# Kernel optimization log

Hardware: AMD Instinct MI355X
Metric: run time of the kernel (lower is better)

The kernel has to match this reference:

```python
import jax, jax.numpy as jnp
import numpy as np
import math

B, LC, LQ, D = 64, 1024, 128, 128


def setup_inputs() -> dict:
    key = jax.random.key(0)
    k1, k2, k3, k4, k5 = jax.random.split(key, 5)
    c_rep = jax.random.normal(k1, (B, LC, D), dtype=jnp.float32)
    q_rep = jax.random.normal(k2, (B, LQ, D), dtype=jnp.float32)
    c_mask = jax.random.randint(k3, (B, LC), 0, 2, dtype=jnp.int32)
    q_mask = jax.random.randint(k4, (B, LQ), 0, 2, dtype=jnp.int32)
    lim = math.sqrt(1.0 / D)
    w = jax.random.uniform(k5, (3 * D,), dtype=jnp.float32, minval=-lim, maxval=lim)
    return {"c_rep": c_rep, "q_rep": q_rep, "c_mask": c_mask, "q_mask": q_mask, "w": w}


def _mask_logits(t, m):
    # mask == 1 means masked (matches original: target*(1-mask) + mask*-1e30)
    return t * (1.0 - m) + m * (-1e30)


def reference(c_rep, q_rep, c_mask, q_mask, w):
    d = c_rep.shape[-1]
    w1, w2, w3 = w[:d], w[d:2 * d], w[2 * d:]
    # Trilinear similarity S[b,i,j] = <ct,w1> + <qt,w2> + <ct*qt,w3>
    # computed without materializing the [B,Lc,Lq,3D] concat tensor.
    S = (c_rep @ w1)[:, :, None] \
        + (q_rep @ w2)[:, None, :] \
        + jnp.einsum('bid,bjd->bij', c_rep * w3, q_rep)  # [B, Lc, Lq]
    qm = q_mask[:, None, :].astype(S.dtype)  # [B, 1, Lq]
    cm = c_mask[:, :, None].astype(S.dtype)  # [B, Lc, 1]
    S1 = jax.nn.softmax(_mask_logits(S, qm), axis=2)  # softmax over query dim
    S2 = jax.nn.softmax(_mask_logits(S, cm), axis=1)  # softmax over context dim
    A = jnp.einsum('bij,bjd->bid', S1, q_rep)  # [B, Lc, D]
    # B_att = S1 @ S2^T @ c_rep, associated right-first to avoid [B,Lc,Lc]
    T = jnp.einsum('bkj,bkd->bjd', S2, c_rep)  # [B, Lq, D]
    B_att = jnp.einsum('bij,bjd->bid', S1, T)  # [B, Lc, D]
    out = jnp.concatenate([c_rep, A, c_rep * A, c_rep * B_att], axis=2)  # [B, Lc, 4D]
    # dropout is identity at inference
    return out
```

## Files before the change

### kernel.cpp

```cpp
#include <hip/hip_runtime.h>
#include <hip/hip_bf16.h>
#include <cstdint>
#include <cstddef>

#define B_   64
#define LC_  1024
#define LQ_  128
#define D_   128

typedef __bf16 bf16;
typedef bf16  bf16x8 __attribute__((ext_vector_type(8)));
typedef bf16  bf16x4 __attribute__((ext_vector_type(4)));
typedef float f32x4  __attribute__((ext_vector_type(4)));

__device__ __forceinline__ f32x4 mfma16(bf16x8 a, bf16x8 b, f32x4 c) {
  return __builtin_amdgcn_mfma_f32_16x16x32_bf16(a, b, c, 0, 0, 0);
}

__global__ __launch_bounds__(256) void k0c(const float* __restrict__ c, const float* __restrict__ w,
                                           float* __restrict__ cw1, bf16* __restrict__ cw3,
                                           bf16* __restrict__ cT) {
  __shared__ float w1s[128];
  __shared__ float w3s[128];
  __shared__ bf16  ctile[128 * 132];
  const int b = blockIdx.y, ks = blockIdx.x;
  const int k0 = ks * 128;
  const int t = threadIdx.x;
  if (t < 128) { w1s[t] = w[t]; w3s[t] = w[256 + t]; }
  __syncthreads();
  {
    const int r = t >> 1, d0 = (t & 1) * 64;
    const float* crow = c + ((size_t)(b * LC_ + k0 + r) * D_ + d0);
    bf16* orow = cw3 + ((size_t)(b * LC_ + k0 + r) * D_ + d0);
    float dot = 0.f;
#pragma unroll
    for (int v = 0; v < 8; ++v) {
      const float4 f0 = ((const float4*)crow)[v * 2 + 0];
      const float4 f1 = ((const float4*)crow)[v * 2 + 1];
      const int dd = d0 + v * 8;
      dot += f0.x * w1s[dd + 0] + f0.y * w1s[dd + 1] + f0.z * w1s[dd + 2] + f0.w * w1s[dd + 3]
           + f1.x * w1s[dd + 4] + f1.y * w1s[dd + 5] + f1.z * w1s[dd + 6] + f1.w * w1s[dd + 7];
      bf16* cr = &ctile[r * 132 + dd];
      cr[0] = (bf16)f0.x; cr[1] = (bf16)f0.y; cr[2] = (bf16)f0.z; cr[3] = (bf16)f0.w;
      cr[4] = (bf16)f1.x; cr[5] = (bf16)f1.y; cr[6] = (bf16)f1.z; cr[7] = (bf16)f1.w;
      bf16x8 o;
      o[0] = (bf16)(f0.x * w3s[dd + 0]); o[1] = (bf16)(f0.y * w3s[dd + 1]);
      o[2] = (bf16)(f0.z * w3s[dd + 2]); o[3] = (bf16)(f0.w * w3s[dd + 3]);
      o[4] = (bf16)(f1.x * w3s[dd + 4]); o[5] = (bf16)(f1.y * w3s[dd + 5]);
      o[6] = (bf16)(f1.z * w3s[dd + 6]); o[7] = (bf16)(f1.w * w3s[dd + 7]);
      *(bf16x8*)(orow + v * 8) = o;
    }
    dot += __shfl_xor(dot, 1);
    if ((t & 1) == 0) cw1[b * LC_ + k0 + r] = dot;
  }
  __syncthreads();
  {
    const int d = t >> 1, kh = (t & 1) * 64;
    bf16* trow = cT + ((size_t)(b * D_ + d) * LC_ + k0 + kh);
#pragma unroll
    for (int v = 0; v < 8; ++v) {
      bf16x8 o;
#pragma unroll
      for (int e = 0; e < 8; ++e) o[e] = ctile[(kh + v * 8 + e) * 132 + d];
      *(bf16x8*)(trow + v * 8) = o;
    }
  }
}

__global__ __launch_bounds__(256) void k0q(const float* __restrict__ q, const float* __restrict__ w,
                                           float* __restrict__ qw2, bf16* __restrict__ qb,
                                           bf16* __restrict__ qT) {
  __shared__ float w2s[128];
  __shared__ bf16  qtile[128 * 132];
  const int b = blockIdx.x;
  const int t = threadIdx.x;
  if (t < 128) w2s[t] = w[128 + t];
  __syncthreads();
  {
    const int r = t >> 1, d0 = (t & 1) * 64;
    const float* qrow = q + ((size_t)(b * LQ_ + r) * D_ + d0);
    bf16* orow = qb + ((size_t)(b * LQ_ + r) * D_ + d0);
    float dot = 0.f;
#pragma unroll
    for (int v = 0; v < 8; ++v) {
      const float4 f0 = ((const float4*)qrow)[v * 2 + 0];
      const float4 f1 = ((const float4*)qrow)[v * 2 + 1];
      const int dd = d0 + v * 8;
      dot += f0.x * w2s[dd + 0] + f0.y * w2s[dd + 1] + f0.z * w2s[dd + 2] + f0.w * w2s[dd + 3]
           + f1.x * w2s[dd + 4] + f1.y * w2s[dd + 5] + f1.z * w2s[dd + 6] + f1.w * w2s[dd + 7];
      bf16x8 o;
      o[0] = (bf16)f0.x; o[1] = (bf16)f0.y; o[2] = (bf16)f0.z; o[3] = (bf16)f0.w;
      o[4] = (bf16)f1.x; o[5] = (bf16)f1.y; o[6] = (bf16)f1.z; o[7] = (bf16)f1.w;
      bf16* qr = &qtile[r * 132 + dd];
#pragma unroll
      for (int e = 0; e < 8; ++e) qr[e] = o[e];
      *(bf16x8*)(orow + v * 8) = o;
    }
    dot += __shfl_xor(dot, 1);
    if ((t & 1) == 0) qw2[b * LQ_ + r] = dot;
  }
  __syncthreads();
  {
    const int d = t >> 1, jh = (t & 1) * 64;
    bf16* trow = qT + ((size_t)(b * D_ + d) * LQ_ + jh);
#pragma unroll
    for (int v = 0; v < 8; ++v) {
      bf16x8 o;
#pragma unroll
      for (int e = 0; e < 8; ++e) o[e] = qtile[(jh + v * 8 + e) * 132 + d];
      *(bf16x8*)(trow + v * 8) = o;
    }
  }
}

__global__ __launch_bounds__(256) void k1p(const float* __restrict__ cw1, const float* __restrict__ qw2,
                                           const int* __restrict__ cmask,
                                           const bf16* __restrict__ cw3, const bf16* __restrict__ cT,
                                           const bf16* __restrict__ qb,
                                           float* __restrict__ Tpart, float* __restrict__ lpart) {
  __shared__ bf16  qs[32 * 136];
  __shared__ bf16  cw3t[64 * 136];
  __shared__ bf16  cTt[128 * 72];
  __shared__ bf16  PT[32 * 72];
  __shared__ float lred[4][32];
  const int bx = blockIdx.x;
  const int ks = bx >> 2, js = bx & 3;
  const int b = blockIdx.y;
  const int j0 = js * 32;
  const int t = threadIdx.x;
  const int w = t >> 6, lane = t & 63, quad = lane >> 4, l15 = lane & 15;

#pragma unroll
  for (int idx = t; idx < 512; idx += 256) {
    const int row = idx >> 4, ch = idx & 15;
    *(bf16x8*)&qs[row * 136 + ch * 8] =
        *(const bf16x8*)(qb + ((size_t)(b * LQ_ + j0 + row) * D_ + ch * 8));
  }
  const f32x4 z = {0.f, 0.f, 0.f, 0.f};
  f32x4 Tacc[2][2] = {{z, z}, {z, z}};
  float lacc0 = 0.f, lacc1 = 0.f;
  __syncthreads();

  for (int kt = 0; kt < 8; ++kt) {
    const int k0g = ks * 512 + kt * 64;
#pragma unroll
    for (int idx = t; idx < 1024; idx += 256) {
      const int row = idx >> 4, ch = idx & 15;
      *(bf16x8*)&cw3t[row * 136 + ch * 8] =
          *(const bf16x8*)(cw3 + ((size_t)(b * LC_ + k0g + row) * D_ + ch * 8));
    }
#pragma unroll
    for (int idx = t; idx < 1024; idx += 256) {
      const int row = idx >> 3, ch = idx & 7;
      *(bf16x8*)&cTt[row * 72 + ch * 8] =
          *(const bf16x8*)(cT + ((size_t)(b * D_ + row) * LC_ + k0g + ch * 8));
    }
    __syncthreads();

    f32x4 S0 = z, S1 = z;
#pragma unroll
    for (int kk = 0; kk < 4; ++kk) {
      bf16x8 a  = *(bf16x8*)&cw3t[(w * 16 + l15) * 136 + kk * 32 + quad * 8];
      bf16x8 b0 = *(bf16x8*)&qs[l15 * 136 + kk * 32 + quad * 8];
      bf16x8 b1 = *(bf16x8*)&qs[(16 + l15) * 136 + kk * 32 + quad * 8];
      S0 = mfma16(a, b0, S0);
      S1 = mfma16(a, b1, S1);
    }
    const float qv0 = qw2[b * LQ_ + j0 + l15];
    const float qv1 = qw2[b * LQ_ + j0 + 16 + l15];
    bf16x4 pk0, pk1;
#pragma unroll
    for (int rr = 0; rr < 4; ++rr) {
      const int krow = k0g + w * 16 + quad * 4 + rr;
      const float c1 = cw1[b * LC_ + krow];
      const int   cm = cmask[b * LC_ + krow];
      const float p0 = cm ? 0.f : __expf(S0[rr] + c1 + qv0);
      const float p1 = cm ? 0.f : __expf(S1[rr] + c1 + qv1);
      lacc0 += p0; lacc1 += p1;
      pk0[rr] = (bf16)p0; pk1[rr] = (bf16)p1;
    }
    *(bf16x4*)&PT[l15 * 72 + w * 16 + quad * 4] = pk0;
    *(bf16x4*)&PT[(16 + l15) * 72 + w * 16 + quad * 4] = pk1;
    __syncthreads();

#pragma unroll
    for (int kk = 0; kk < 2; ++kk) {
      bf16x8 a0 = *(bf16x8*)&PT[l15 * 72 + kk * 32 + quad * 8];
      bf16x8 a1 = *(bf16x8*)&PT[(16 + l15) * 72 + kk * 32 + quad * 8];
      bf16x8 b0 = *(bf16x8*)&cTt[(w * 32 + l15) * 72 + kk * 32 + quad * 8];
      bf16x8 b1 = *(bf16x8*)&cTt[(w * 32 + 16 + l15) * 72 + kk * 32 + quad * 8];
      Tacc[0][0] = mfma16(a0, b0, Tacc[0][0]);
      Tacc[0][1] = mfma16(a0, b1, Tacc[0][1]);
      Tacc[1][0] = mfma16(a1, b0, Tacc[1][0]);
      Tacc[1][1] = mfma16(a1, b1, Tacc[1][1]);
    }
    __syncthreads();
  }

  lacc0 += __shfl_xor(lacc0, 16); lacc0 += __shfl_xor(lacc0, 32);
  lacc1 += __shfl_xor(lacc1, 16); lacc1 += __shfl_xor(lacc1, 32);
  if (lane < 16) { lred[w][l15] = lacc0; lred[w][16 + l15] = lacc1; }
  __syncthreads();
  if (t < 32)
    lpart[(size_t)(b * 2 + ks) * 128 + j0 + t] = lred[0][t] + lred[1][t] + lred[2][t] + lred[3][t];

  float* tp = Tpart + ((size_t)((b * 2 + ks) * 4 + js)) * (32 * 128);
#pragma unroll
  for (int mt = 0; mt < 2; ++mt)
#pragma unroll
    for (int nt = 0; nt < 2; ++nt)
#pragma unroll
      for (int rr = 0; rr < 4; ++rr)
        tp[(mt * 16 + quad * 4 + rr) * 128 + w * 32 + nt * 16 + l15] = Tacc[mt][nt][rr];
}

__global__ __launch_bounds__(256) void k1r(const float* __restrict__ Tpart,
                                           const float* __restrict__ lpart,
                                           bf16* __restrict__ TT) {
  __shared__ float Tsum[32 * 132];
  __shared__ float linv[32];
  const int js = blockIdx.x, b = blockIdx.y;
  const int j0 = js * 32;
  const int t = threadIdx.x;
  const float4* p0 = (const float4*)(Tpart + ((size_t)((b * 2 + 0) * 4 + js)) * (32 * 128));
  const float4* p1 = (const float4*)(Tpart + ((size_t)((b * 2 + 1) * 4 + js)) * (32 * 128));
#pragma unroll
  for (int idx = t; idx < 1024; idx += 256) {
    const int row = idx >> 5, seg = idx & 31;
    const float4 v0 = p0[idx];
    const float4 v1 = p1[idx];
    float4 s;
    s.x = v0.x + v1.x; s.y = v0.y + v1.y; s.z = v0.z + v1.z; s.w = v0.w + v1.w;
    *(float4*)&Tsum[row * 132 + seg * 4] = s;
  }
  if (t < 32)
    linv[t] = 1.f / (lpart[(size_t)(b * 2 + 0) * 128 + j0 + t] +
                     lpart[(size_t)(b * 2 + 1) * 128 + j0 + t]);
  __syncthreads();
  const int d = t >> 1, jh = (t & 1) * 16;
  bf16x8 o0, o1;
#pragma unroll
  for (int e = 0; e < 8; ++e) {
    o0[e] = (bf16)(Tsum[(jh + e) * 132 + d] * linv[jh + e]);
    o1[e] = (bf16)(Tsum[(jh + 8 + e) * 132 + d] * linv[jh + 8 + e]);
  }
  bf16* dst = TT + ((size_t)(b * D_ + d) * LQ_ + j0 + jh);
  *(bf16x8*)dst = o0;
  *(bf16x8*)(dst + 8) = o1;
}

__global__ __launch_bounds__(256) void k2(const float* __restrict__ c, const float* __restrict__ cw1,
                                          const float* __restrict__ qw2, const int* __restrict__ qmask,
                                          const bf16* __restrict__ cw3, const bf16* __restrict__ qb,
                                          const bf16* __restrict__ qT, const bf16* __restrict__ TT,
                                          float* __restrict__ out) {
  __shared__ __align__(16) char smem[51712];
  bf16* cw3i = (bf16*)(smem);
  bf16* qsl  = (bf16*)(smem + 17408);
  bf16* qTsl = (bf16*)(smem + 26112);
  bf16* TTsl = (bf16*)(smem + 36352);
  bf16* P1   = (bf16*)(smem + 46592);
  float* A32 = (float*)(smem);
  float* B32 = (float*)(smem + 16896);
  const int it = blockIdx.x, b = blockIdx.y;
  const int i0 = it * 64;
  const int t = threadIdx.x;
  const int w = t >> 6, lane = t & 63, quad = lane >> 4, l15 = lane & 15;

#pragma unroll
  for (int idx = t; idx < 1024; idx += 256) {
    const int row = idx >> 4, ch = idx & 15;
    *(bf16x8*)&cw3i[row * 136 + ch * 8] =
        *(const bf16x8*)(cw3 + ((size_t)(b * LC_ + i0 + row) * D_ + ch * 8));
  }
  const f32x4 z = {0.f, 0.f, 0.f, 0.f};
  f32x4 Aacc[8], Bacc[8];
#pragma unroll
  for (int n = 0; n < 8; ++n) { Aacc[n] = z; Bacc[n] = z; }
  float lacc[4] = {0.f, 0.f, 0.f, 0.f};
  __syncthreads();

  for (int jt = 0; jt < 4; ++jt) {
    const int j0 = jt * 32;
#pragma unroll
    for (int idx = t; idx < 512; idx += 256) {
      const int row = idx >> 4, ch = idx & 15;
      *(bf16x8*)&qsl[row * 136 + ch * 8] =
          *(const bf16x8*)(qb + ((size_t)(b * LQ_ + j0 + row) * D_ + ch * 8));
    }
#pragma unroll
    for (int idx = t; idx < 512; idx += 256) {
      const int row = idx >> 2, ch = idx & 3;
      *(bf16x8*)&qTsl[row * 40 + ch * 8] =
          *(const bf16x8*)(qT + ((size_t)(b * D_ + row) * LQ_ + j0 + ch * 8));
    }
#pragma unroll
    for (int idx = t; idx < 512; idx += 256) {
      const int row = idx >> 2, ch = idx & 3;
      *(bf16x8*)&TTsl[row * 40 + ch * 8] =
          *(const bf16x8*)(TT + ((size_t)(b * D_ + row) * LQ_ + j0 + ch * 8));
    }
    __syncthreads();

    f32x4 S0 = z, S1 = z;
#pragma unroll
    for (int kk = 0; kk < 4; ++kk) {
      bf16x8 a  = *(bf16x8*)&cw3i[(w * 16 + l15) * 136 + kk * 32 + quad * 8];
      bf16x8 b0 = *(bf16x8*)&qsl[l15 * 136 + kk * 32 + quad * 8];
      bf16x8 b1 = *(bf16x8*)&qsl[(16 + l15) * 136 + kk * 32 + quad * 8];
      S0 = mfma16(a, b0, S0);
      S1 = mfma16(a, b1, S1);
    }
    const float qv0 = qw2[b * LQ_ + j0 + l15];
    const float qv1 = qw2[b * LQ_ + j0 + 16 + l15];
    const int   qm0 = qmask[b * LQ_ + j0 + l15];
    const int   qm1 = qmask[b * LQ_ + j0 + 16 + l15];
#pragma unroll
    for (int rr = 0; rr < 4; ++rr) {
      const int irow = i0 + w * 16 + quad * 4 + rr;
      const float c1 = cw1[b * LC_ + irow];
      const float p0 = qm0 ? 0.f : __expf(S0[rr] + c1 + qv0);
      const float p1 = qm1 ? 0.f : __expf(S1[rr] + c1 + qv1);
      lacc[rr] += p0 + p1;
      P1[(w * 16 + quad * 4 + rr) * 40 + l15] = (bf16)p0;
      P1[(w * 16 + quad * 4 + rr) * 40 + 16 + l15] = (bf16)p1;
    }
    __syncthreads();

    bf16x8 aP = *(bf16x8*)&P1[(w * 16 + l15) * 40 + quad * 8];
#pragma unroll
    for (int nt = 0; nt < 8; ++nt) {
      bf16x8 bq = *(bf16x8*)&qTsl[(nt * 16 + l15) * 40 + quad * 8];
      bf16x8 bt = *(bf16x8*)&TTsl[(nt * 16 + l15) * 40 + quad * 8];
      Aacc[nt] = mfma16(aP, bq, Aacc[nt]);
      Bacc[nt] = mfma16(aP, bt, Bacc[nt]);
    }
    __syncthreads();
  }

#pragma unroll
  for (int rr = 0; rr < 4; ++rr) {
    float v = lacc[rr];
    v += __shfl_xor(v, 1); v += __shfl_xor(v, 2);
    v += __shfl_xor(v, 4); v += __shfl_xor(v, 8);
    lacc[rr] = 1.f / v;
  }

#pragma unroll
  for (int h = 0; h < 2; ++h) {
    if ((w >> 1) == h) {
      const int lrow0 = (w & 1) * 16 + quad * 4;
#pragma unroll
      for (int nt = 0; nt < 8; ++nt)
#pragma unroll
        for (int rr = 0; rr < 4; ++rr) {
          A32[(lrow0 + rr) * 132 + nt * 16 + l15] = Aacc[nt][rr] * lacc[rr];
          B32[(lrow0 + rr) * 132 + nt * 16 + l15] = Bacc[nt][rr] * lacc[rr];
        }
    }
    __syncthreads();
#pragma unroll
    for (int idx = t; idx < 1024; idx += 256) {
      const int lrow = idx >> 5, seg = idx & 31;
      const size_t grow = (size_t)(b * LC_ + i0 + h * 32 + lrow);
      const float4 c4 = ((const float4*)(c + grow * D_))[seg];
      const float4 a4 = *(float4*)&A32[lrow * 132 + seg * 4];
      const float4 b4 = *(float4*)&B32[lrow * 132 + seg * 4];
      float4* ob = (float4*)(out + grow * 512);
      ob[seg] = c4;
      ob[32 + seg] = a4;
      float4 ca; ca.x = c4.x * a4.x; ca.y = c4.y * a4.y; ca.z = c4.z * a4.z; ca.w = c4.w * a4.w;
      ob[64 + seg] = ca;
      float4 cb; cb.x = c4.x * b4.x; cb.y = c4.y * b4.y; cb.z = c4.z * b4.z; cb.w = c4.w * b4.w;
      ob[96 + seg] = cb;
    }
    __syncthreads();
  }
}

extern "C" void kernel_launch(void* const* d_in, const int* in_sizes, int n_in,
                              void* d_out, int out_size, void* d_ws, size_t ws_size,
                              hipStream_t stream) {
  (void)in_sizes; (void)n_in; (void)out_size; (void)ws_size;
  const float* c     = (const float*)d_in[0];
  const float* q     = (const float*)d_in[1];
  const int*   cmask = (const int*)d_in[2];
  const int*   qmask = (const int*)d_in[3];
  const float* w     = (const float*)d_in[4];
  float* out = (float*)d_out;

  char* ws = (char*)d_ws;
  float* cw1 = (float*)(ws + 0);
  float* qw2 = (float*)(ws + 262144);
  bf16*  cw3 = (bf16*)(ws + 294912);
  bf16*  cT  = (bf16*)(ws + 17072128);
  bf16*  qb  = (bf16*)(ws + 33849344);
  bf16*  qT  = (bf16*)(ws + 35946496);
  bf16*  TT  = (bf16*)(ws + 38043648);

  float* Tpart = out;
  float* lpart = out + 2097152;

  k0c<<<dim3(8, 64), 256, 0, stream>>>(c, w, cw1, cw3, cT);
  k0q<<<dim3(64), 256, 0, stream>>>(q, w, qw2, qb, qT);
  k1p<<<dim3(8, 64), 256, 0, stream>>>(cw1, qw2, cmask, cw3, cT, qb, Tpart, lpart);
  k1r<<<dim3(4, 64), 256, 0, stream>>>(Tpart, lpart, TT);
  k2<<<dim3(16, 64), 256, 0, stream>>>(c, cw1, qw2, qmask, cw3, qb, qT, TT, out);
}
```

Baseline: 246.8 us.

## Merge prep kernels, load MFMA operands directly from global, split context wider

Fuses the context and query preprocessing kernels into one launch with a branch on block index. In k1p and k2, operand tiles are no longer staged in LDS; each lane loads its MFMA fragments straight from global memory (L2-resident bf16), cutting LDS usage and barriers and allowing launch_bounds occupancy hints of 4. k1p now splits the context dimension four ways instead of two, doubling the grid, and the reduction kernel sums four partials. The cost is uncoalesced, repeated global fragment loads that depend on caches, and larger partial buffers.

```diff
diff --git a/kernel.cpp b/kernel.cpp
--- a/kernel.cpp
+++ b/kernel.cpp
@@ -17,110 +17,102 @@
   return __builtin_amdgcn_mfma_f32_16x16x32_bf16(a, b, c, 0, 0, 0);
 }
 
-__global__ __launch_bounds__(256) void k0c(const float* __restrict__ c, const float* __restrict__ w,
-                                           float* __restrict__ cw1, bf16* __restrict__ cw3,
-                                           bf16* __restrict__ cT) {
-  __shared__ float w1s[128];
-  __shared__ float w3s[128];
-  __shared__ bf16  ctile[128 * 132];
-  const int b = blockIdx.y, ks = blockIdx.x;
-  const int k0 = ks * 128;
+__global__ __launch_bounds__(256) void k0(const float* __restrict__ c, const float* __restrict__ q,
+                                          const float* __restrict__ w,
+                                          float* __restrict__ cw1, float* __restrict__ qw2,
+                                          bf16* __restrict__ cw3, bf16* __restrict__ cT,
+                                          bf16* __restrict__ qb, bf16* __restrict__ qT) {
+  __shared__ float wbuf[256];
+  __shared__ bf16  tile[128 * 132];
+  const int b = blockIdx.y;
   const int t = threadIdx.x;
-  if (t < 128) { w1s[t] = w[t]; w3s[t] = w[256 + t]; }
-  __syncthreads();
-  {
-    const int r = t >> 1, d0 = (t & 1) * 64;
-    const float* crow = c + ((size_t)(b * LC_ + k0 + r) * D_ + d0);
-    bf16* orow = cw3 + ((size_t)(b * LC_ + k0 + r) * D_ + d0);
-    float dot = 0.f;
-#pragma unroll
-    for (int v = 0; v < 8; ++v) {
-      const float4 f0 = ((const float4*)crow)[v * 2 + 0];
-      const float4 f1 = ((const float4*)crow)[v * 2 + 1];
-      const int dd = d0 + v * 8;
-      dot += f0.x * w1s[dd + 0] + f0.y * w1s[dd + 1] + f0.z * w1s[dd + 2] + f0.w * w1s[dd + 3]
-           + f1.x * w1s[dd + 4] + f1.y * w1s[dd + 5] + f1.z * w1s[dd + 6] + f1.w * w1s[dd + 7];
-      bf16* cr = &ctile[r * 132 + dd];
-      cr[0] = (bf16)f0.x; cr[1] = (bf16)f0.y; cr[2] = (bf16)f0.z; cr[3] = (bf16)f0.w;
-      cr[4] = (bf16)f1.x; cr[5] = (bf16)f1.y; cr[6] = (bf16)f1.z; cr[7] = (bf16)f1.w;
-      bf16x8 o;
-      o[0] = (bf16)(f0.x * w3s[dd + 0]); o[1] = (bf16)(f0.y * w3s[dd + 1]);
-      o[2] = (bf16)(f0.z * w3s[dd + 2]); o[3] = (bf16)(f0.w * w3s[dd + 3]);
-      o[4] = (bf16)(f1.x * w3s[dd + 4]); o[5] = (bf16)(f1.y * w3s[dd + 5]);
-      o[6] = (bf16)(f1.z * w3s[dd + 6]); o[7] = (bf16)(f1.w * w3s[dd + 7]);
-      *(bf16x8*)(orow + v * 8) = o;
-    }
-    dot += __shfl_xor(dot, 1);
-    if ((t & 1) == 0) cw1[b * LC_ + k0 + r] = dot;
-  }
-  __syncthreads();
-  {
-    const int d = t >> 1, kh = (t & 1) * 64;
-    bf16* trow = cT + ((size_t)(b * D_ + d) * LC_ + k0 + kh);
-#pragma unroll
-    for (int v = 0; v < 8; ++v) {
-      bf16x8 o;
-#pragma unroll
-      for (int e = 0; e < 8; ++e) o[e] = ctile[(kh + v * 8 + e) * 132 + d];
-      *(bf16x8*)(trow + v * 8) = o;
-    }
-  }
-}
-
-__global__ __launch_bounds__(256) void k0q(const float* __restrict__ q, const float* __restrict__ w,
-                                           float* __restrict__ qw2, bf16* __restrict__ qb,
-                                           bf16* __restrict__ qT) {
-  __shared__ float w2s[128];
-  __shared__ bf16  qtile[128 * 132];
-  const int b = blockIdx.x;
-  const int t = threadIdx.x;
-  if (t < 128) w2s[t] = w[128 + t];
-  __syncthreads();
-  {
-    const int r = t >> 1, d0 = (t & 1) * 64;
-    const float* qrow = q + ((size_t)(b * LQ_ + r) * D_ + d0);
-    bf16* orow = qb + ((size_t)(b * LQ_ + r) * D_ + d0);
-    float dot = 0.f;
-#pragma unroll
-    for (int v = 0; v < 8; ++v) {
-      const float4 f0 = ((const float4*)qrow)[v * 2 + 0];
-      const float4 f1 = ((const float4*)qrow)[v * 2 + 1];
-      const int dd = d0 + v * 8;
-      dot += f0.x * w2s[dd + 0] + f0.y * w2s[dd + 1] + f0.z * w2s[dd + 2] + f0.w * w2s[dd + 3]
-           + f1.x * w2s[dd + 4] + f1.y * w2s[dd + 5] + f1.z * w2s[dd + 6] + f1.w * w2s[dd + 7];
-      bf16x8 o;
-      o[0] = (bf16)f0.x; o[1] = (bf16)f0.y; o[2] = (bf16)f0.z; o[3] = (bf16)f0.w;
-      o[4] = (bf16)f1.x; o[5] = (bf16)f1.y; o[6] = (bf16)f1.z; o[7] = (bf16)f1.w;
-      bf16* qr = &qtile[r * 132 + dd];
-#pragma unroll
-      for (int e = 0; e < 8; ++e) qr[e] = o[e];
-      *(bf16x8*)(orow + v * 8) = o;
-    }
-    dot += __shfl_xor(dot, 1);
-    if ((t & 1) == 0) qw2[b * LQ_ + r] = dot;
-  }
-  __syncthreads();
-  {
-    const int d = t >> 1, jh = (t & 1) * 64;
-    bf16* trow = qT + ((size_t)(b * D_ + d) * LQ_ + jh);
-#pragma unroll
-    for (int v = 0; v < 8; ++v) {
-      bf16x8 o;
-#pragma unroll
-      for (int e = 0; e < 8; ++e) o[e] = qtile[(jh + v * 8 + e) * 132 + d];
-      *(bf16x8*)(trow + v * 8) = o;
-    }
-  }
-}
-
-__global__ __launch_bounds__(256) void k1p(const float* __restrict__ cw1, const float* __restrict__ qw2,
-                                           const int* __restrict__ cmask,
-                                           const bf16* __restrict__ cw3, const bf16* __restrict__ cT,
-                                           const bf16* __restrict__ qb,
-                                           float* __restrict__ Tpart, float* __restrict__ lpart) {
-  __shared__ bf16  qs[32 * 136];
-  __shared__ bf16  cw3t[64 * 136];
-  __shared__ bf16  cTt[128 * 72];
+  if (blockIdx.x < 8) {
+    const int k0 = blockIdx.x * 128;
+    if (t < 128) { wbuf[t] = w[t]; wbuf[128 + t] = w[256 + t]; }
+    __syncthreads();
+    {
+      const int r = t >> 1, d0 = (t & 1) * 64;
+      const float* crow = c + ((size_t)(b * LC_ + k0 + r) * D_ + d0);
+      bf16* orow = cw3 + ((size_t)(b * LC_ + k0 + r) * D_ + d0);
+      float dot = 0.f;
+#pragma unroll
+      for (int v = 0; v < 8; ++v) {
+        const float4 f0 = ((const float4*)crow)[v * 2 + 0];
+        const float4 f1 = ((const float4*)crow)[v * 2 + 1];
+        const int dd = d0 + v * 8;
+        dot += f0.x * wbuf[dd + 0] + f0.y * wbuf[dd + 1] + f0.z * wbuf[dd + 2] + f0.w * wbuf[dd + 3]
+             + f1.x * wbuf[dd + 4] + f1.y * wbuf[dd + 5] + f1.z * wbuf[dd + 6] + f1.w * wbuf[dd + 7];
+        bf16* cr = &tile[r * 132 + dd];
+        cr[0] = (bf16)f0.x; cr[1] = (bf16)f0.y; cr[2] = (bf16)f0.z; cr[3] = (bf16)f0.w;
+        cr[4] = (bf16)f1.x; cr[5] = (bf16)f1.y; cr[6] = (bf16)f1.z; cr[7] = (bf16)f1.w;
+        bf16x8 o;
+        o[0] = (bf16)(f0.x * wbuf[128 + dd + 0]); o[1] = (bf16)(f0.y * wbuf[128 + dd + 1]);
+        o[2] = (bf16)(f0.z * wbuf[128 + dd + 2]); o[3] = (bf16)(f0.w * wbuf[128 + dd + 3]);
+        o[4] = (bf16)(f1.x * wbuf[128 + dd + 4]); o[5] = (bf16)(f1.y * wbuf[128 + dd + 5]);
+        o[6] = (bf16)(f1.z * wbuf[128 + dd + 6]); o[7] = (bf16)(f1.w * wbuf[128 + dd + 7]);
+        *(bf16x8*)(orow + v * 8) = o;
+      }
+      dot += __shfl_xor(dot, 1);
+      if ((t & 1) == 0) cw1[b * LC_ + k0 + r] = dot;
+    }
+    __syncthreads();
+    {
+      const int d = t >> 1, kh = (t & 1) * 64;
+      bf16* trow = cT + ((size_t)(b * D_ + d) * LC_ + k0 + kh);
+#pragma unroll
+      for (int v = 0; v < 8; ++v) {
+        bf16x8 o;
+#pragma unroll
+        for (int e = 0; e < 8; ++e) o[e] = tile[(kh + v * 8 + e) * 132 + d];
+        *(bf16x8*)(trow + v * 8) = o;
+      }
+    }
+  } else {
+    if (t < 128) wbuf[t] = w[128 + t];
+    __syncthreads();
+    {
+      const int r = t >> 1, d0 = (t & 1) * 64;
+      const float* qrow = q + ((size_t)(b * LQ_ + r) * D_ + d0);
+      bf16* orow = qb + ((size_t)(b * LQ_ + r) * D_ + d0);
+      float dot = 0.f;
+#pragma unroll
+      for (int v = 0; v < 8; ++v) {
+        const float4 f0 = ((const float4*)qrow)[v * 2 + 0];
+        const float4 f1 = ((const float4*)qrow)[v * 2 + 1];
+        const int dd = d0 + v * 8;
+        dot += f0.x * wbuf[dd + 0] + f0.y * wbuf[dd + 1] + f0.z * wbuf[dd + 2] + f0.w * wbuf[dd + 3]
+             + f1.x * wbuf[dd + 4] + f1.y * wbuf[dd + 5] + f1.z * wbuf[dd + 6] + f1.w * wbuf[dd + 7];
+        bf16x8 o;
+        o[0] = (bf16)f0.x; o[1] = (bf16)f0.y; o[2] = (bf16)f0.z; o[3] = (bf16)f0.w;
+        o[4] = (bf16)f1.x; o[5] = (bf16)f1.y; o[6] = (bf16)f1.z; o[7] = (bf16)f1.w;
+        bf16* qr = &tile[r * 132 + dd];
+#pragma unroll
+        for (int e = 0; e < 8; ++e) qr[e] = o[e];
+        *(bf16x8*)(orow + v * 8) = o;
+      }
+      dot += __shfl_xor(dot, 1);
+      if ((t & 1) == 0) qw2[b * LQ_ + r] = dot;
+    }
+    __syncthreads();
+    {
+      const int d = t >> 1, jh = (t & 1) * 64;
+      bf16* trow = qT + ((size_t)(b * D_ + d) * LQ_ + jh);
+#pragma unroll
+      for (int v = 0; v < 8; ++v) {
+        bf16x8 o;
+#pragma unroll
+        for (int e = 0; e < 8; ++e) o[e] = tile[(jh + v * 8 + e) * 132 + d];
+        *(bf16x8*)(trow + v * 8) = o;
+      }
+    }
+  }
+}
+
+__global__ __launch_bounds__(256, 4) void k1p(const float* __restrict__ cw1, const float* __restrict__ qw2,
+                                              const int* __restrict__ cmask,
+                                              const bf16* __restrict__ cw3, const bf16* __restrict__ cT,
+                                              const bf16* __restrict__ qb,
+                                              float* __restrict__ Tpart, float* __restrict__ lpart) {
   __shared__ bf16  PT[32 * 72];
   __shared__ float lred[4][32];
   const int bx = blockIdx.x;
@@ -130,44 +122,27 @@
   const int t = threadIdx.x;
   const int w = t >> 6, lane = t & 63, quad = lane >> 4, l15 = lane & 15;
 
-#pragma unroll
-  for (int idx = t; idx < 512; idx += 256) {
-    const int row = idx >> 4, ch = idx & 15;
-    *(bf16x8*)&qs[row * 136 + ch * 8] =
-        *(const bf16x8*)(qb + ((size_t)(b * LQ_ + j0 + row) * D_ + ch * 8));
-  }
+  bf16x8 bq[4][2];
+#pragma unroll
+  for (int kk = 0; kk < 4; ++kk) {
+    bq[kk][0] = *(const bf16x8*)(qb + ((size_t)(b * LQ_ + j0 + l15) * D_ + kk * 32 + quad * 8));
+    bq[kk][1] = *(const bf16x8*)(qb + ((size_t)(b * LQ_ + j0 + 16 + l15) * D_ + kk * 32 + quad * 8));
+  }
+  const float qv0 = qw2[b * LQ_ + j0 + l15];
+  const float qv1 = qw2[b * LQ_ + j0 + 16 + l15];
   const f32x4 z = {0.f, 0.f, 0.f, 0.f};
   f32x4 Tacc[2][2] = {{z, z}, {z, z}};
   float lacc0 = 0.f, lacc1 = 0.f;
-  __syncthreads();
-
-  for (int kt = 0; kt < 8; ++kt) {
-    const int k0g = ks * 512 + kt * 64;
-#pragma unroll
-    for (int idx = t; idx < 1024; idx += 256) {
-      const int row = idx >> 4, ch = idx & 15;
-      *(bf16x8*)&cw3t[row * 136 + ch * 8] =
-          *(const bf16x8*)(cw3 + ((size_t)(b * LC_ + k0g + row) * D_ + ch * 8));
-    }
-#pragma unroll
-    for (int idx = t; idx < 1024; idx += 256) {
-      const int row = idx >> 3, ch = idx & 7;
-      *(bf16x8*)&cTt[row * 72 + ch * 8] =
-          *(const bf16x8*)(cT + ((size_t)(b * D_ + row) * LC_ + k0g + ch * 8));
-    }
-    __syncthreads();
-
+
+  for (int kt = 0; kt < 4; ++kt) {
+    const int k0g = ks * 256 + kt * 64;
     f32x4 S0 = z, S1 = z;
 #pragma unroll
     for (int kk = 0; kk < 4; ++kk) {
-      bf16x8 a  = *(bf16x8*)&cw3t[(w * 16 + l15) * 136 + kk * 32 + quad * 8];
-      bf16x8 b0 = *(bf16x8*)&qs[l15 * 136 + kk * 32 + quad * 8];
-      bf16x8 b1 = *(bf16x8*)&qs[(16 + l15) * 136 + kk * 32 + quad * 8];
-      S0 = mfma16(a, b0, S0);
-      S1 = mfma16(a, b1, S1);
-    }
-    const float qv0 = qw2[b * LQ_ + j0 + l15];
-    const float qv1 = qw2[b * LQ_ + j0 + 16 + l15];
+      bf16x8 a = *(const bf16x8*)(cw3 + ((size_t)(b * LC_ + k0g + w * 16 + l15) * D_ + kk * 32 + quad * 8));
+      S0 = mfma16(a, bq[kk][0], S0);
+      S1 = mfma16(a, bq[kk][1], S1);
+    }
     bf16x4 pk0, pk1;
 #pragma unroll
     for (int rr = 0; rr < 4; ++rr) {
@@ -187,8 +162,8 @@
     for (int kk = 0; kk < 2; ++kk) {
       bf16x8 a0 = *(bf16x8*)&PT[l15 * 72 + kk * 32 + quad * 8];
       bf16x8 a1 = *(bf16x8*)&PT[(16 + l15) * 72 + kk * 32 + quad * 8];
-      bf16x8 b0 = *(bf16x8*)&cTt[(w * 32 + l15) * 72 + kk * 32 + quad * 8];
-      bf16x8 b1 = *(bf16x8*)&cTt[(w * 32 + 16 + l15) * 72 + kk * 32 + quad * 8];
+      bf16x8 b0 = *(const bf16x8*)(cT + ((size_t)(b * D_ + w * 32 + l15) * LC_ + k0g + kk * 32 + quad * 8));
+      bf16x8 b1 = *(const bf16x8*)(cT + ((size_t)(b * D_ + w * 32 + 16 + l15) * LC_ + k0g + kk * 32 + quad * 8));
       Tacc[0][0] = mfma16(a0, b0, Tacc[0][0]);
       Tacc[0][1] = mfma16(a0, b1, Tacc[0][1]);
       Tacc[1][0] = mfma16(a1, b0, Tacc[1][0]);
@@ -202,9 +177,9 @@
   if (lane < 16) { lred[w][l15] = lacc0; lred[w][16 + l15] = lacc1; }
   __syncthreads();
   if (t < 32)
-    lpart[(size_t)(b * 2 + ks) * 128 + j0 + t] = lred[0][t] + lred[1][t] + lred[2][t] + lred[3][t];
-
-  float* tp = Tpart + ((size_t)((b * 2 + ks) * 4 + js)) * (32 * 128);
+    lpart[(size_t)(b * 4 + ks) * 128 + j0 + t] = lred[0][t] + lred[1][t] + lred[2][t] + lred[3][t];
+
+  float* tp = Tpart + ((size_t)((b * 4 + ks) * 4 + js)) * (32 * 128);
 #pragma unroll
   for (int mt = 0; mt < 2; ++mt)
 #pragma unroll
@@ -222,20 +197,29 @@
   const int js = blockIdx.x, b = blockIdx.y;
   const int j0 = js * 32;
   const int t = threadIdx.x;
-  const float4* p0 = (const float4*)(Tpart + ((size_t)((b * 2 + 0) * 4 + js)) * (32 * 128));
-  const float4* p1 = (const float4*)(Tpart + ((size_t)((b * 2 + 1) * 4 + js)) * (32 * 128));
+  const float4* p0 = (const float4*)(Tpart + ((size_t)((b * 4 + 0) * 4 + js)) * (32 * 128));
+  const float4* p1 = (const float4*)(Tpart + ((size_t)((b * 4 + 1) * 4 + js)) * (32 * 128));
+  const float4* p2 = (const float4*)(Tpart + ((size_t)((b * 4 + 2) * 4 + js)) * (32 * 128));
+  const float4* p3 = (const float4*)(Tpart + ((size_t)((b * 4 + 3) * 4 + js)) * (32 * 128));
 #pragma unroll
   for (int idx = t; idx < 1024; idx += 256) {
     const int row = idx >> 5, seg = idx & 31;
     const float4 v0 = p0[idx];
     const float4 v1 = p1[idx];
+    const float4 v2 = p2[idx];
+    const float4 v3 = p3[idx];
     float4 s;
-    s.x = v0.x + v1.x; s.y = v0.y + v1.y; s.z = v0.z + v1.z; s.w = v0.w + v1.w;
+    s.x = (v0.x + v1.x) + (v2.x + v3.x);
+    s.y = (v0.y + v1.y) + (v2.y + v3.y);
+    s.z = (v0.z + v1.z) + (v2.z + v3.z);
+    s.w = (v0.w + v1.w) + (v2.w + v3.w);
     *(float4*)&Tsum[row * 132 + seg * 4] = s;
   }
   if (t < 32)
-    linv[t] = 1.f / (lpart[(size_t)(b * 2 + 0) * 128 + j0 + t] +
-                     lpart[(size_t)(b * 2 + 1) * 128 + j0 + t]);
+    linv[t] = 1.f / (lpart[(size_t)(b * 4 + 0) * 128 + j0 + t] +
+                     lpart[(size_t)(b * 4 + 1) * 128 + j0 + t] +
+                     lpart[(size_t)(b * 4 + 2) * 128 + j0 + t] +
+                     lpart[(size_t)(b * 4 + 3) * 128 + j0 + t]);
   __syncthreads();
   const int d = t >> 1, jh = (t & 1) * 16;
   bf16x8 o0, o1;
@@ -249,67 +233,44 @@
   *(bf16x8*)(dst + 8) = o1;
 }
 
-__global__ __launch_bounds__(256) void k2(const float* __restrict__ c, const float* __restrict__ cw1,
-                                          const float* __restrict__ qw2, const int* __restrict__ qmask,
-                                          const bf16* __restrict__ cw3, const bf16* __restrict__ qb,
-                                          const bf16* __restrict__ qT, const bf16* __restrict__ TT,
-                                          float* __restrict__ out) {
-  __shared__ __align__(16) char smem[51712];
-  bf16* cw3i = (bf16*)(smem);
-  bf16* qsl  = (bf16*)(smem + 17408);
-  bf16* qTsl = (bf16*)(smem + 26112);
-  bf16* TTsl = (bf16*)(smem + 36352);
-  bf16* P1   = (bf16*)(smem + 46592);
-  float* A32 = (float*)(smem);
+__global__ __launch_bounds__(256, 4) void k2(const float* __restrict__ c, const float* __restrict__ cw1,
+                                             const float* __restrict__ qw2, const int* __restrict__ qmask,
+                                             const bf16* __restrict__ cw3, const bf16* __restrict__ qb,
+                                             const bf16* __restrict__ qT, const bf16* __restrict__ TT,
+                                             float* __restrict__ out) {
+  __shared__ __align__(16) char smem[33792];
+  bf16*  P1  = (bf16*)smem;
+  float* A32 = (float*)smem;
   float* B32 = (float*)(smem + 16896);
   const int it = blockIdx.x, b = blockIdx.y;
   const int i0 = it * 64;
   const int t = threadIdx.x;
   const int w = t >> 6, lane = t & 63, quad = lane >> 4, l15 = lane & 15;
 
-#pragma unroll
-  for (int idx = t; idx < 1024; idx += 256) {
-    const int row = idx >> 4, ch = idx & 15;
-    *(bf16x8*)&cw3i[row * 136 + ch * 8] =
-        *(const bf16x8*)(cw3 + ((size_t)(b * LC_ + i0 + row) * D_ + ch * 8));
-  }
+  bf16x8 af[4];
+#pragma unroll
+  for (int kk = 0; kk < 4; ++kk)
+    af[kk] = *(const bf16x8*)(cw3 + ((size_t)(b * LC_ + i0 + w * 16 + l15) * D_ + kk * 32 + quad * 8));
+  float c1r[4];
+#pragma unroll
+  for (int rr = 0; rr < 4; ++rr)
+    c1r[rr] = cw1[b * LC_ + i0 + w * 16 + quad * 4 + rr];
+
   const f32x4 z = {0.f, 0.f, 0.f, 0.f};
   f32x4 Aacc[8], Bacc[8];
 #pragma unroll
   for (int n = 0; n < 8; ++n) { Aacc[n] = z; Bacc[n] = z; }
   float lacc[4] = {0.f, 0.f, 0.f, 0.f};
-  __syncthreads();
 
   for (int jt = 0; jt < 4; ++jt) {
     const int j0 = jt * 32;
-#pragma unroll
-    for (int idx = t; idx < 512; idx += 256) {
-      const int row = idx >> 4, ch = idx & 15;
-      *(bf16x8*)&qsl[row * 136 + ch * 8] =
-          *(const bf16x8*)(qb + ((size_t)(b * LQ_ + j0 + row) * D_ + ch * 8));
-    }
-#pragma unroll
-    for (int idx = t; idx < 512; idx += 256) {
-      const int row = idx >> 2, ch = idx & 3;
-      *(bf16x8*)&qTsl[row * 40 + ch * 8] =
-          *(const bf16x8*)(qT + ((size_t)(b * D_ + row) * LQ_ + j0 + ch * 8));
-    }
-#pragma unroll
-    for (int idx = t; idx < 512; idx += 256) {
-      const int row = idx >> 2, ch = idx & 3;
-      *(bf16x8*)&TTsl[row * 40 + ch * 8] =
-          *(const bf16x8*)(TT + ((size_t)(b * D_ + row) * LQ_ + j0 + ch * 8));
-    }
-    __syncthreads();
-
     f32x4 S0 = z, S1 = z;
 #pragma unroll
     for (int kk = 0; kk < 4; ++kk) {
-      bf16x8 a  = *(bf16x8*)&cw3i[(w * 16 + l15) * 136 + kk * 32 + quad * 8];
-      bf16x8 b0 = *(bf16x8*)&qsl[l15 * 136 + kk * 32 + quad * 8];
-      bf16x8 b1 = *(bf16x8*)&qsl[(16 + l15) * 136 + kk * 32 + quad * 8];
-      S0 = mfma16(a, b0, S0);
-      S1 = mfma16(a, b1, S1);
+      bf16x8 b0 = *(const bf16x8*)(qb + ((size_t)(b * LQ_ + j0 + l15) * D_ + kk * 32 + quad * 8));
+      bf16x8 b1 = *(const bf16x8*)(qb + ((size_t)(b * LQ_ + j0 + 16 + l15) * D_ + kk * 32 + quad * 8));
+      S0 = mfma16(af[kk], b0, S0);
+      S1 = mfma16(af[kk], b1, S1);
     }
     const float qv0 = qw2[b * LQ_ + j0 + l15];
     const float qv1 = qw2[b * LQ_ + j0 + 16 + l15];
@@ -317,10 +278,8 @@
     const int   qm1 = qmask[b * LQ_ + j0 + 16 + l15];
 #pragma unroll
     for (int rr = 0; rr < 4; ++rr) {
-      const int irow = i0 + w * 16 + quad * 4 + rr;
-      const float c1 = cw1[b * LC_ + irow];
-      const float p0 = qm0 ? 0.f : __expf(S0[rr] + c1 + qv0);
-      const float p1 = qm1 ? 0.f : __expf(S1[rr] + c1 + qv1);
+      const float p0 = qm0 ? 0.f : __expf(S0[rr] + c1r[rr] + qv0);
+      const float p1 = qm1 ? 0.f : __expf(S1[rr] + c1r[rr] + qv1);
       lacc[rr] += p0 + p1;
       P1[(w * 16 + quad * 4 + rr) * 40 + l15] = (bf16)p0;
       P1[(w * 16 + quad * 4 + rr) * 40 + 16 + l15] = (bf16)p1;
@@ -330,10 +289,10 @@
     bf16x8 aP = *(bf16x8*)&P1[(w * 16 + l15) * 40 + quad * 8];
 #pragma unroll
     for (int nt = 0; nt < 8; ++nt) {
-      bf16x8 bq = *(bf16x8*)&qTsl[(nt * 16 + l15) * 40 + quad * 8];
-      bf16x8 bt = *(bf16x8*)&TTsl[(nt * 16 + l15) * 40 + quad * 8];
-      Aacc[nt] = mfma16(aP, bq, Aacc[nt]);
-      Bacc[nt] = mfma16(aP, bt, Bacc[nt]);
+      bf16x8 bq2 = *(const bf16x8*)(qT + ((size_t)(b * D_ + nt * 16 + l15) * LQ_ + j0 + quad * 8));
+      bf16x8 bt2 = *(const bf16x8*)(TT + ((size_t)(b * D_ + nt * 16 + l15) * LQ_ + j0 + quad * 8));
+      Aacc[nt] = mfma16(aP, bq2, Aacc[nt]);
+      Bacc[nt] = mfma16(aP, bt2, Bacc[nt]);
     }
     __syncthreads();
   }
@@ -399,11 +358,10 @@
   bf16*  TT  = (bf16*)(ws + 38043648);
 
   float* Tpart = out;
-  float* lpart = out + 2097152;
-
-  k0c<<<dim3(8, 64), 256, 0, stream>>>(c, w, cw1, cw3, cT);
-  k0q<<<dim3(64), 256, 0, stream>>>(q, w, qw2, qb, qT);
-  k1p<<<dim3(8, 64), 256, 0, stream>>>(cw1, qw2, cmask, cw3, cT, qb, Tpart, lpart);
+  float* lpart = out + 4194304;
+
+  k0 <<<dim3(9, 64), 256, 0, stream>>>(c, q, w, cw1, qw2, cw3, cT, qb, qT);
+  k1p<<<dim3(16, 64), 256, 0, stream>>>(cw1, qw2, cmask, cw3, cT, qb, Tpart, lpart);
   k1r<<<dim3(4, 64), 256, 0, stream>>>(Tpart, lpart, TT);
-  k2<<<dim3(16, 64), 256, 0, stream>>>(c, cw1, qw2, qmask, cw3, qb, qT, TT, out);
-}
+  k2 <<<dim3(16, 64), 256, 0, stream>>>(c, cw1, qw2, qmask, cw3, qb, qT, TT, out);
+}
```

Result: slower. 288.3 us (+16.8%).
